# Performance work log

Hardware: AMD Instinct MI355X
Metric: run time of the kernel (lower is better)

## Reference

```python
import jax, jax.numpy as jnp
import numpy as np

N = 4096
IN, HID, OUT = 512, 512, 512
EMB, MHID = 64, 128
GRID_SIZE, SPLINE_ORDER = 5, 3
D_B = GRID_SIZE + SPLINE_ORDER + 1      # 9
SPLINE_DIM = GRID_SIZE + SPLINE_ORDER   # 8


def make_grid():
    h = (1.0 - (-1.0)) / GRID_SIZE
    return jnp.arange(-SPLINE_ORDER, GRID_SIZE + SPLINE_ORDER + 1, dtype=jnp.float32) * h - 1.0


def b_splines(x, grid):
    # x: (N, in) -> (N, in, SPLINE_DIM); Cox-de Boor recursion, epsilon-stabilized
    xg = x[..., None]
    bases = ((xg >= grid[:-1]) & (xg < grid[1:])).astype(x.dtype)
    eps = 1e-08
    for k in range(1, SPLINE_ORDER + 1):
        dp = grid[k:-1] - grid[:-(k + 1)]
        dn = grid[k + 1:] - grid[1:-k]
        bases = (xg - grid[:-(k + 1)]) / (dp + eps) * bases[..., :-1] \
              + (grid[k + 1:] - xg) / (dn + eps) * bases[..., 1:]
    return bases


def _xavier(k, shape):
    fan_out, fan_in = shape
    std = (2.0 / (fan_in + fan_out)) ** 0.5
    return std * jax.random.normal(k, shape, jnp.float32)


def setup_inputs() -> dict:
    key = jax.random.key(0)
    ks = jax.random.split(key, 7)
    x = 2.0 * jax.random.uniform(ks[0], (N, IN), jnp.float32) - 1.0
    inp = {"x": x}
    dims = [(IN, HID), (HID, OUT)]
    for i, (fi, fo) in enumerate(dims):
        kk = jax.random.split(ks[i + 1], 3)
        inp[f"emb{i}"] = _xavier(kk[0], (fi * fo, EMB))   # layout: (out, in) flattened, out outer
        inp[f"w1_{i}"] = _xavier(kk[1], (MHID, EMB))
        inp[f"b1_{i}"] = jnp.zeros((MHID,), jnp.float32)
        inp[f"w2_{i}"] = _xavier(kk[2], (D_B, MHID))
        inp[f"b2_{i}"] = jnp.zeros((D_B,), jnp.float32)
    return inp


def _kan_layer(h, emb, w1, b1, w2, b2, in_f, out_f, grid):
    basis = b_splines(h, grid)                              # (N, in, SPLINE_DIM)
    w = (emb @ w1.T + b1) @ w2.T + b2                       # (out*in, D_B)
    w = w.reshape(out_f, in_f, D_B)
    w_spline = w[..., :SPLINE_DIM]                          # (out, in, SPLINE_DIM)
    w_base = w[..., SPLINE_DIM]                             # (out, in)  == weights[:, :, -1]
    out = jnp.einsum('nis,ois->no', basis, w_spline)
    out = out + jnp.einsum('ni,oi->no', jax.nn.silu(h), w_base)
    return out


def reference(x, emb0, w1_0, b1_0, w2_0, b2_0, emb1, w1_1, b1_1, w2_1, b2_1):
    grid = make_grid()
    h = _kan_layer(x, emb0, w1_0, b1_0, w2_0, b2_0, IN, HID, grid)
    h = _kan_layer(h, emb1, w1_1, b1_1, w2_1, b2_1, HID, OUT, grid)
    return h
```

## Files before the change

kernel.cpp:

```cpp
#include <hip/hip_runtime.h>
#include <cstdint>
#include <cstddef>

typedef unsigned short u16;
typedef unsigned int   u32;

typedef __bf16 bf16x8 __attribute__((ext_vector_type(8)));
typedef float  f32x4  __attribute__((ext_vector_type(4)));

#define NROWS 4096
#define INF   512
#define OUTF  512
#define EMB   64
#define MHID  128
#define DB    9
#define KDIM  (INF * DB)
#define MN    (NROWS * OUTF)

__device__ __forceinline__ u16 f2bf(float f) {
    union { float f; u32 ui; } v; v.f = f;
    u32 u = v.ui;
    u += 0x7fffu + ((u >> 16) & 1u);
    return (u16)(u >> 16);
}
__device__ __forceinline__ float gridv(int t) { return (float)(t - 3) * 0.4f - 1.0f; }

__global__ __launch_bounds__(256) void meff_kernel(
    const float* __restrict__ w1_0, const float* __restrict__ b1_0,
    const float* __restrict__ w2_0, const float* __restrict__ b2_0,
    const float* __restrict__ w1_1, const float* __restrict__ b1_1,
    const float* __restrict__ w2_1, const float* __restrict__ b2_1,
    float* __restrict__ Mc)
{
    int tid  = threadIdx.x;
    int lane = tid & 63;
    int wid  = blockIdx.x * 4 + (tid >> 6);
    if (wid >= 1170) return;
    int layer = wid / 585;
    int o     = wid % 585;
    const float* w1 = layer ? w1_1 : w1_0;
    const float* b1 = layer ? b1_1 : b1_0;
    const float* w2 = layer ? w2_1 : w2_0;
    const float* b2 = layer ? b2_1 : b2_0;

    float p;
    int d;
    if (o < 576) {
        int j = o / 9; d = o % 9;
        p = w1[lane * EMB + j]        * w2[d * MHID + lane]
          + w1[(lane + 64) * EMB + j] * w2[d * MHID + lane + 64];
    } else {
        d = o - 576;
        p = b1[lane] * w2[d * MHID + lane] + b1[lane + 64] * w2[d * MHID + lane + 64];
    }
#pragma unroll
    for (int off = 32; off >= 1; off >>= 1)
        p += __shfl_xor(p, off, 64);
    if (lane == 0) {
        if (o >= 576) p += b2[d];
        Mc[layer * 1024 + o] = p;
    }
}

__global__ __launch_bounds__(256, 4) void genw_kernel(
    const float* __restrict__ emb0, const float* __restrict__ emb1,
    const float* __restrict__ Mc,
    u16* __restrict__ Bw0, u16* __restrict__ Bw1)
{
    __shared__ __align__(16) u16 ob[256 * 9];
    int layer = blockIdx.y;
    const float* emb = layer ? emb1 : emb0;
    u16* Bw = layer ? Bw1 : Bw0;
    const float* mc = Mc + layer * 1024;

    int tid = threadIdx.x;
    size_t row = (size_t)blockIdx.x * 256 + tid;

    const float4* g4 = (const float4*)(emb + row * EMB);
    float4 v[16];
#pragma unroll
    for (int j = 0; j < 16; ++j) v[j] = g4[j];

    float acc[9];
#pragma unroll
    for (int d = 0; d < 9; ++d) acc[d] = mc[576 + d];

#pragma unroll
    for (int jj = 0; jj < 16; ++jj) {
#pragma unroll
        for (int d = 0; d < 9; ++d)
            acc[d] += v[jj].x * mc[(jj * 4 + 0) * 9 + d]
                    + v[jj].y * mc[(jj * 4 + 1) * 9 + d]
                    + v[jj].z * mc[(jj * 4 + 2) * 9 + d]
                    + v[jj].w * mc[(jj * 4 + 3) * 9 + d];
    }

#pragma unroll
    for (int d = 0; d < 9; ++d) ob[tid * 9 + d] = f2bf(acc[d]);
    __syncthreads();

    const uint4* src = (const uint4*)ob;
    uint4* dst = (uint4*)(Bw + (size_t)blockIdx.x * 256 * 9);
    for (int s = tid; s < 288; s += 256) dst[s] = src[s];
}

__global__ __launch_bounds__(256) void phi_kernel(const float* __restrict__ xin,
                                                  const float* __restrict__ part,
                                                  int S,
                                                  u16* __restrict__ phi)
{
    __shared__ __align__(16) u16 lbuf[256 * 9];
    int tid = threadIdx.x;
    int idx = blockIdx.x * 256 + tid;

    float xv;
    if (part) {
        xv = 0.f;
        for (int z = 0; z < S; ++z) xv += part[(size_t)z * MN + idx];
    } else {
        xv = xin[idx];
    }

    float b[11];
#pragma unroll
    for (int t = 0; t < 11; ++t)
        b[t] = (xv >= gridv(t) && xv < gridv(t + 1)) ? 1.0f : 0.0f;
#pragma unroll
    for (int k = 1; k <= 3; ++k) {
#pragma unroll
        for (int t = 0; t + k < 11; ++t) {
            float rdp = 1.0f / ((gridv(t + k) - gridv(t)) + 1e-8f);
            float rdn = 1.0f / ((gridv(t + k + 1) - gridv(t + 1)) + 1e-8f);
            b[t] = (xv - gridv(t)) * rdp * b[t] + (gridv(t + k + 1) - xv) * rdn * b[t + 1];
        }
    }
    float sil = xv / (1.0f + expf(-xv));

#pragma unroll
    for (int d = 0; d < 8; ++d) lbuf[tid * 9 + d] = f2bf(b[d]);
    lbuf[tid * 9 + 8] = f2bf(sil);
    __syncthreads();

    const uint4* src = (const uint4*)lbuf;
    uint4* dst = (uint4*)(phi + (size_t)blockIdx.x * 256 * 9);
    for (int s = tid; s < 288; s += 256) dst[s] = src[s];
}

#define GLOAD16(gp, lp) __builtin_amdgcn_global_load_lds(                         \
    (const __attribute__((address_space(1))) u32*)(gp),                           \
    (__attribute__((address_space(3))) u32*)(lp), 16, 0, 0)

__global__ __launch_bounds__(256, 4) void gemm_kernel(const __bf16* __restrict__ A,
                                                      const __bf16* __restrict__ B,
                                                      float* __restrict__ Cpart,
                                                      int N, int K, int ksz)
{
    __shared__ __align__(16) __bf16 As[128 * 64];
    __shared__ __align__(16) __bf16 Bs[128 * 64];

    int tid  = threadIdx.x;
    int lane = tid & 63;
    int wv   = tid >> 6;
    int wm   = wv >> 1, wn = wv & 1;
    int brow = blockIdx.x * 128;
    int bcol = blockIdx.y * 128;
    int z    = blockIdx.z;
    int kbeg = z * ksz, kend = kbeg + ksz;

    f32x4 acc[4][4];
#pragma unroll
    for (int r = 0; r < 4; ++r)
#pragma unroll
        for (int c = 0; c < 4; ++c)
#pragma unroll
            for (int g = 0; g < 4; ++g) acc[r][c][g] = 0.0f;

    int quad = lane >> 4;
    int l16  = lane & 15;

    for (int k0 = kbeg; k0 < kend; k0 += 64) {
#pragma unroll
        for (int q = 0; q < 4; ++q) {
            int chunk = q * 256 + wv * 64 + lane;
            int row   = chunk >> 3;
            int slot  = chunk & 7;
            int col   = ((slot ^ (row & 7)) << 3);
            const __bf16* ga = A + (size_t)(brow + row) * K + (k0 + col);
            const __bf16* gb = B + (size_t)(bcol + row) * K + (k0 + col);
            GLOAD16(ga, &As[(q * 256 + wv * 64) * 8]);
            GLOAD16(gb, &Bs[(q * 256 + wv * 64) * 8]);
        }
        __syncthreads();

#pragma unroll
        for (int ks = 0; ks < 2; ++ks) {
            bf16x8 af[4], bfr[4];
#pragma unroll
            for (int r = 0; r < 4; ++r) {
                int arow = wm * 64 + r * 16 + l16;
                af[r] = *(const bf16x8*)&As[arow * 64 + (((ks * 4 + quad) ^ (arow & 7)) << 3)];
                int brw = wn * 64 + r * 16 + l16;
                bfr[r] = *(const bf16x8*)&Bs[brw * 64 + (((ks * 4 + quad) ^ (brw & 7)) << 3)];
            }
#pragma unroll
            for (int r = 0; r < 4; ++r)
#pragma unroll
                for (int c = 0; c < 4; ++c)
                    acc[r][c] = __builtin_amdgcn_mfma_f32_16x16x32_bf16(af[r], bfr[c], acc[r][c], 0, 0, 0);
        }
        __syncthreads();
    }

    float* Cz = Cpart + (size_t)z * MN;
#pragma unroll
    for (int r = 0; r < 4; ++r)
#pragma unroll
        for (int c = 0; c < 4; ++c)
#pragma unroll
            for (int g = 0; g < 4; ++g) {
                int grow = brow + wm * 64 + r * 16 + quad * 4 + g;
                int gcol = bcol + wn * 64 + c * 16 + l16;
                Cz[(size_t)grow * N + gcol] = acc[r][c][g];
            }
}

__global__ __launch_bounds__(256) void reduce_kernel(const float* __restrict__ part,
                                                     int S, float* __restrict__ out)
{
    int i = blockIdx.x * 256 + threadIdx.x;
    const float4* p4 = (const float4*)part;
    float4 s = p4[i];
    for (int z = 1; z < S; ++z) {
        float4 v = p4[(size_t)z * (MN / 4) + i];
        s.x += v.x; s.y += v.y; s.z += v.z; s.w += v.w;
    }
    ((float4*)out)[i] = s;
}

extern "C" void kernel_launch(void* const* d_in, const int* in_sizes, int n_in,
                              void* d_out, int out_size, void* d_ws, size_t ws_size,
                              hipStream_t stream)
{
    const float* x    = (const float*)d_in[0];
    const float* emb0 = (const float*)d_in[1];
    const float* w1_0 = (const float*)d_in[2];
    const float* b1_0 = (const float*)d_in[3];
    const float* w2_0 = (const float*)d_in[4];
    const float* b2_0 = (const float*)d_in[5];
    const float* emb1 = (const float*)d_in[6];
    const float* w1_1 = (const float*)d_in[7];
    const float* b1_1 = (const float*)d_in[8];
    const float* w2_1 = (const float*)d_in[9];
    const float* b2_1 = (const float*)d_in[10];

    char* ws = (char*)d_ws;
    const size_t PHI_OFF  = 0;
    const size_t BW0_OFF  = 37748736;
    const size_t BW1_OFF  = BW0_OFF + 4718592;
    const size_t MC_OFF   = BW1_OFF + 4718592;
    const size_t PART_OFF = MC_OFF + 8192;

    int S = 1;
    const size_t SLAB = 8388608ull;
    if      (ws_size >= PART_OFF + 4 * SLAB) S = 4;
    else if (ws_size >= PART_OFF + 2 * SLAB) S = 2;
    int ksz = KDIM / S;

    u16*   phi  = (u16*)(ws + PHI_OFF);
    u16*   Bw0  = (u16*)(ws + BW0_OFF);
    u16*   Bw1  = (u16*)(ws + BW1_OFF);
    float* Mc   = (float*)(ws + MC_OFF);
    float* part = (float*)(ws + PART_OFF);

    meff_kernel<<<293, 256, 0, stream>>>(w1_0, b1_0, w2_0, b2_0,
                                         w1_1, b1_1, w2_1, b2_1, Mc);
    genw_kernel<<<dim3(1024, 2), 256, 0, stream>>>(emb0, emb1, Mc, Bw0, Bw1);

    phi_kernel<<<8192, 256, 0, stream>>>(x, nullptr, 0, phi);
    gemm_kernel<<<dim3(32, 4, S), 256, 0, stream>>>((const __bf16*)phi, (const __bf16*)Bw0,
                                                    part, OUTF, KDIM, ksz);
    phi_kernel<<<8192, 256, 0, stream>>>(nullptr, part, S, phi);
    gemm_kernel<<<dim3(32, 4, S), 256, 0, stream>>>((const __bf16*)phi, (const __bf16*)Bw1,
                                                    part, OUTF, KDIM, ksz);
    reduce_kernel<<<2048, 256, 0, stream>>>(part, S, (float*)d_out);
}
```

Before: 274.3 us.

## Coalesce embedding loads in genw via lane-split dot products and shuffle reduction

The weight-generation kernel now has each wavefront read 64 embedding rows as contiguous float4s. Each group of 16 lanes holds a slice of one row and the matching 36-entry slice of the collapsed MLP matrix in registers. Partial 9-wide dot products are summed with xor-shuffles, and one lane per row writes the bf16 result to shared memory. This replaces the old scheme where each thread loaded its own 256-byte row (strided, uncoalesced) and read the matrix from global memory in the inner loop. The cost is 36 shuffles per 4 rows and a next-load prefetch, and the occupancy hint is dropped from the launch bounds.

```diff
diff --git a/kernel.cpp b/kernel.cpp
--- a/kernel.cpp
+++ b/kernel.cpp
@@ -62,7 +62,7 @@
     }
 }
 
-__global__ __launch_bounds__(256, 4) void genw_kernel(
+__global__ __launch_bounds__(256) void genw_kernel(
     const float* __restrict__ emb0, const float* __restrict__ emb1,
     const float* __restrict__ Mc,
     u16* __restrict__ Bw0, u16* __restrict__ Bw1)
@@ -73,32 +73,55 @@
     u16* Bw = layer ? Bw1 : Bw0;
     const float* mc = Mc + layer * 1024;
 
-    int tid = threadIdx.x;
-    size_t row = (size_t)blockIdx.x * 256 + tid;
-
-    const float4* g4 = (const float4*)(emb + row * EMB);
-    float4 v[16];
-#pragma unroll
-    for (int j = 0; j < 16; ++j) v[j] = g4[j];
-
-    float acc[9];
-#pragma unroll
-    for (int d = 0; d < 9; ++d) acc[d] = mc[576 + d];
-
-#pragma unroll
-    for (int jj = 0; jj < 16; ++jj) {
+    int tid  = threadIdx.x;
+    int lane = tid & 63;
+    int w    = tid >> 6;
+    int cg   = lane & 15;
+    int rg   = lane >> 4;
+
+    float M[36];
+    {
+        const float4* m4 = (const float4*)(mc + cg * 36);
+#pragma unroll
+        for (int q = 0; q < 9; ++q) {
+            float4 t = m4[q];
+            M[q * 4 + 0] = t.x; M[q * 4 + 1] = t.y;
+            M[q * 4 + 2] = t.z; M[q * 4 + 3] = t.w;
+        }
+    }
+    float c9[9];
+#pragma unroll
+    for (int d = 0; d < 9; ++d) c9[d] = mc[576 + d];
+
+    size_t base_row = (size_t)blockIdx.x * 256 + (size_t)w * 64;
+    const float4* g4 = (const float4*)(emb + base_row * EMB);
+
+    float4 vc = g4[lane];
+#pragma unroll
+    for (int i = 0; i < 16; ++i) {
+        float4 vn;
+        if (i < 15) vn = g4[(i + 1) * 64 + lane];
+
+        float p[9];
 #pragma unroll
         for (int d = 0; d < 9; ++d)
-            acc[d] += v[jj].x * mc[(jj * 4 + 0) * 9 + d]
-                    + v[jj].y * mc[(jj * 4 + 1) * 9 + d]
-                    + v[jj].z * mc[(jj * 4 + 2) * 9 + d]
-                    + v[jj].w * mc[(jj * 4 + 3) * 9 + d];
-    }
-
-#pragma unroll
-    for (int d = 0; d < 9; ++d) ob[tid * 9 + d] = f2bf(acc[d]);
+            p[d] = vc.x * M[d] + vc.y * M[9 + d] + vc.z * M[18 + d] + vc.w * M[27 + d];
+
+#pragma unroll
+        for (int s = 1; s <= 8; s <<= 1)
+#pragma unroll
+            for (int d = 0; d < 9; ++d)
+                p[d] += __shfl_xor(p[d], s, 64);
+
+        if (cg == 0) {
+            int r = w * 64 + i * 4 + rg;
+#pragma unroll
+            for (int d = 0; d < 9; ++d) ob[r * 9 + d] = f2bf(p[d] + c9[d]);
+        }
+        vc = vn;
+    }
+
     __syncthreads();
-
     const uint4* src = (const uint4*)ob;
     uint4* dst = (uint4*)(Bw + (size_t)blockIdx.x * 256 * 9);
     for (int s = tid; s < 288; s += 256) dst[s] = src[s];
```

After: 273.2 us. About the same (-0.4%).
